# Optimization experiments

Hardware: AMD Instinct MI355X
Metric: run time of the kernel (lower is better)

## Reference

```python
import jax, jax.numpy as jnp
import numpy as np

MARGIN = 0.3  # hard-coded in all three MarginRankingLoss instances


def setup_inputs() -> dict:
    key = jax.random.key(0)
    k1, k2, k3, k4 = jax.random.split(key, 4)
    n, d, num_ids = 4096, 2048, 100
    inputs = jax.random.normal(k1, (n, d), dtype=jnp.float32)
    targets_a = jax.random.randint(k2, (n,), 0, num_ids, dtype=jnp.int64)
    targets_b = jax.random.randint(k3, (n,), 0, num_ids, dtype=jnp.int64)
    lam = jax.random.uniform(k4, (), dtype=jnp.float32)
    epoch = 60
    return {"inputs": inputs, "targets_a": targets_a, "targets_b": targets_b,
            "lam": lam, "epoch": epoch}


def reference(inputs, targets_a, targets_b, lam, epoch):
    # pairwise euclidean distance: dist[i,j] = ||x_i - x_j||
    sq = jnp.sum(inputs * inputs, axis=1)                      # [n]
    dist = sq[:, None] + sq[None, :] - 2.0 * (inputs @ inputs.T)
    dist = jnp.sqrt(jnp.clip(dist, 1e-12))                     # [n, n]

    ma = targets_a[:, None] == targets_a[None, :]
    mb = targets_b[:, None] == targets_b[None, :]
    m_same_ab = ma & mb                                        # same a AND b (incl. diagonal)
    m_same_or = (ma & ~mb) | (~ma & mb)                        # exactly one of a/b matches
    m_dif_ab = ~ma & ~mb                                       # neither matches

    ninf = -jnp.inf
    pinf = jnp.inf
    hp = jnp.max(jnp.where(m_same_ab, dist, ninf), axis=1)     # hardest positive
    hn = jnp.min(jnp.where(m_dif_ab, dist, pinf), axis=1)      # hardest negative
    max_or = jnp.max(jnp.where(m_same_or, dist, ninf), axis=1)
    min_or = jnp.min(jnp.where(m_same_or, dist, pinf), axis=1)

    use_or = m_same_or.any(axis=1) & (epoch > 50)
    sp = jnp.where(use_or, max_or, hp)
    sn = jnp.where(use_or, min_or, hn)

    # MarginRankingLoss(x1, x2, y=1) = mean(relu(x2 - x1 + margin))
    loss_1 = jnp.mean(jnp.maximum(0.0, hp - hn + MARGIN))
    loss_2 = jnp.mean(jnp.maximum(0.0, sp - hn + MARGIN))
    loss_3 = jnp.mean(jnp.maximum(0.0, hp - sn + MARGIN))
    return loss_1 + loss_2 + loss_3
```

## Files before the change

kernel.cpp:

```cpp
#include <hip/hip_runtime.h>
#include <hip/hip_bf16.h>

#define NROW 4096
#define KDIM 2048
#define ROWB (KDIM * 2)
#define BT 256
#define BK 64
#define NT (KDIM / BK)
#define LDSBUF 65536
#define PHI(r) (((r) & 7) << 4)

typedef __attribute__((ext_vector_type(8))) short bf16x8;
typedef __attribute__((ext_vector_type(4))) float f32x4;
typedef __attribute__((ext_vector_type(4))) unsigned short u16x4;

#define MFMA16(a, b, c) __builtin_amdgcn_mfma_f32_16x16x32_bf16((a), (b), (c), 0, 0, 0)

__device__ __forceinline__ unsigned short f2bf(float x) {
    unsigned u = __float_as_uint(x);
    unsigned r = (u + 0x7FFFu + ((u >> 16) & 1u)) >> 16;
    return (unsigned short)r;
}
__device__ __forceinline__ float bf2f(unsigned short b) {
    return __uint_as_float(((unsigned)b) << 16);
}

__global__ __launch_bounds__(256) void k_convert(const float* __restrict__ X,
                                                 unsigned short* __restrict__ Xb,
                                                 float* __restrict__ sqv) {
    const int row = blockIdx.x;
    const int t = threadIdx.x;
    const float4* xr = (const float4*)(X + (size_t)row * KDIM);
    unsigned short* br = Xb + (size_t)row * KDIM;
    float acc = 0.f;
#pragma unroll
    for (int it = 0; it < 2; ++it) {
        int idx = t * 2 + it;
        float4 v = xr[idx];
        u16x4 b;
        b.x = f2bf(v.x); b.y = f2bf(v.y); b.z = f2bf(v.z); b.w = f2bf(v.w);
        float f0 = bf2f(b.x), f1 = bf2f(b.y), f2 = bf2f(b.z), f3 = bf2f(b.w);
        acc += f0 * f0 + f1 * f1 + f2 * f2 + f3 * f3;
        *(u16x4*)(br + idx * 4) = b;
    }
#pragma unroll
    for (int s = 32; s > 0; s >>= 1) acc += __shfl_xor(acc, s);
    __shared__ float red[4];
    const int lane = t & 63, wid = t >> 6;
    if (lane == 0) red[wid] = acc;
    __syncthreads();
    if (t == 0) sqv[row] = red[0] + red[1] + red[2] + red[3];
}

__global__ __launch_bounds__(256) void k_init(unsigned* hp, unsigned* hn,
                                              unsigned* mor, unsigned* mir,
                                              int* anyor, float* out) {
    int i = blockIdx.x * 256 + threadIdx.x;
    hp[i] = 0u;
    hn[i] = 0x7F800000u;
    mor[i] = 0u;
    mir[i] = 0x7F800000u;
    anyor[i] = 0;
    if (i == 0) out[0] = 0.f;
}

__global__ __launch_bounds__(512, 2) void k_gemm(const unsigned short* __restrict__ Xb,
                                                 const float* __restrict__ sqv,
                                                 const int* __restrict__ ta,
                                                 const int* __restrict__ tb,
                                                 unsigned int* __restrict__ hp,
                                                 unsigned int* __restrict__ hn,
                                                 unsigned int* __restrict__ mor,
                                                 unsigned int* __restrict__ mir,
                                                 int* __restrict__ anyor) {
    __shared__ char lds[2 * LDSBUF];
    const int bi = blockIdx.x >> 4;
    const int bj = blockIdx.x & 15;
    const int t = threadIdx.x;
    const int lane = t & 63;
    const int w = t >> 6;
    const int wm = w >> 2;
    const int wn = w & 3;
    const int l15 = lane & 15;
    const int kg16 = (lane >> 4) * 16;
    const char* xbase = (const char*)Xb;

    const int P = (l15 & 7) << 4;
    int akb[2], bkb[2];
#pragma unroll
    for (int ks = 0; ks < 2; ++ks) {
        const int kx = (ks * 64 + kg16) ^ P;
        akb[ks] = (wm * 128 + l15) * 128 + kx;
        bkb[ks] = 32768 + (wn * 64 + l15) * 128 + kx;
    }

    f32x4 acc[8][4] = {};

#define STAGE(tt, p)                                                          \
    do {                                                                      \
        constexpr int isb_ = (p) >= 4;                                        \
        constexpr int c_ = (p) - isb_ * 4;                                    \
        const int row_ = c_ * 64 + (t >> 3);                                  \
        const int gr_ = (isb_ ? bj : bi) * BT + row_;                         \
        const char* gsrc_ = xbase + (size_t)gr_ * ROWB + (size_t)(tt) * 128 + \
                            (((t & 7) * 16) ^ PHI(row_));                     \
        char* ldst_ = lds + ((tt) & 1) * LDSBUF + isb_ * 32768 + row_ * 128 + \
                      (t & 7) * 16;                                           \
        __builtin_amdgcn_global_load_lds(                                     \
            (const __attribute__((address_space(1))) void*)gsrc_,             \
            (__attribute__((address_space(3))) void*)ldst_, 16, 0, 0);        \
    } while (0)

    STAGE(0, 0); STAGE(0, 2); STAGE(0, 4); STAGE(0, 5);
    STAGE(0, 6); STAGE(0, 7); STAGE(0, 1); STAGE(0, 3);
    asm volatile("s_waitcnt vmcnt(2)" ::: "memory");
    __builtin_amdgcn_s_barrier();

    bf16x8 af0[4][2], af1[4][2], b01[2][2], b23[2][2];
#pragma unroll
    for (int ks = 0; ks < 2; ++ks) {
#pragma unroll
        for (int m = 0; m < 4; ++m)
            af0[m][ks] = *(const bf16x8*)(lds + akb[ks] + m * 2048);
        b01[0][ks] = *(const bf16x8*)(lds + bkb[ks]);
        b01[1][ks] = *(const bf16x8*)(lds + bkb[ks] + 2048);
    }

    for (int tk = 0; tk < NT; ++tk) {
        const char* bufc = lds + (tk & 1) * LDSBUF;
        const char* bufn = lds + ((tk + 1) & 1) * LDSBUF;
        const bool stg = (tk + 1) < NT;

        if (stg) {
            STAGE(tk + 1, 0); STAGE(tk + 1, 2); STAGE(tk + 1, 4);
            STAGE(tk + 1, 5); STAGE(tk + 1, 6); STAGE(tk + 1, 7);
        }
#pragma unroll
        for (int ks = 0; ks < 2; ++ks) {
            b23[0][ks] = *(const bf16x8*)(bufc + bkb[ks] + 2 * 2048);
            b23[1][ks] = *(const bf16x8*)(bufc + bkb[ks] + 3 * 2048);
        }
        __builtin_amdgcn_s_setprio(1);
#pragma unroll
        for (int ks = 0; ks < 2; ++ks)
#pragma unroll
            for (int m = 0; m < 4; ++m) {
                acc[m][0] = MFMA16(af0[m][ks], b01[0][ks], acc[m][0]);
                acc[m][1] = MFMA16(af0[m][ks], b01[1][ks], acc[m][1]);
            }
        __builtin_amdgcn_s_setprio(0);

        if (stg) {
            STAGE(tk + 1, 1); STAGE(tk + 1, 3);
            asm volatile("s_waitcnt vmcnt(8)" ::: "memory");
        } else {
            asm volatile("s_waitcnt vmcnt(0)" ::: "memory");
        }
        __builtin_amdgcn_s_barrier();
#pragma unroll
        for (int ks = 0; ks < 2; ++ks)
#pragma unroll
            for (int m = 0; m < 4; ++m)
                af1[m][ks] = *(const bf16x8*)(bufc + akb[ks] + (4 + m) * 2048);
        __builtin_amdgcn_s_setprio(1);
#pragma unroll
        for (int ks = 0; ks < 2; ++ks)
#pragma unroll
            for (int m = 0; m < 4; ++m) {
                acc[m][2] = MFMA16(af0[m][ks], b23[0][ks], acc[m][2]);
                acc[m][3] = MFMA16(af0[m][ks], b23[1][ks], acc[m][3]);
            }
        __builtin_amdgcn_s_setprio(0);

        if (stg) {
            asm volatile("s_waitcnt vmcnt(2)" ::: "memory");
            __builtin_amdgcn_s_barrier();
#pragma unroll
            for (int ks = 0; ks < 2; ++ks)
#pragma unroll
                for (int m = 0; m < 4; ++m)
                    af0[m][ks] = *(const bf16x8*)(bufn + akb[ks] + m * 2048);
        }
        __builtin_amdgcn_s_setprio(1);
#pragma unroll
        for (int ks = 0; ks < 2; ++ks)
#pragma unroll
            for (int m = 0; m < 4; ++m) {
                acc[4 + m][2] = MFMA16(af1[m][ks], b23[0][ks], acc[4 + m][2]);
                acc[4 + m][3] = MFMA16(af1[m][ks], b23[1][ks], acc[4 + m][3]);
            }
        __builtin_amdgcn_s_setprio(0);

        __builtin_amdgcn_s_setprio(1);
#pragma unroll
        for (int ks = 0; ks < 2; ++ks)
#pragma unroll
            for (int m = 0; m < 4; ++m) {
                acc[4 + m][0] = MFMA16(af1[m][ks], b01[0][ks], acc[4 + m][0]);
                acc[4 + m][1] = MFMA16(af1[m][ks], b01[1][ks], acc[4 + m][1]);
            }
        __builtin_amdgcn_s_setprio(0);
        if (stg) {
#pragma unroll
            for (int ks = 0; ks < 2; ++ks) {
                b01[0][ks] = *(const bf16x8*)(bufn + bkb[ks]);
                b01[1][ks] = *(const bf16x8*)(bufn + bkb[ks] + 2048);
            }
        }
        __builtin_amdgcn_s_barrier();
    }
#undef STAGE

    float sqj[4];
    int taj[4], tbj[4];
#pragma unroll
    for (int n = 0; n < 4; ++n) {
        int j = bj * BT + wn * 64 + n * 16 + l15;
        sqj[n] = sqv[j];
        taj[n] = ta[j];
        tbj[n] = tb[j];
    }
    const float INF = __uint_as_float(0x7F800000u);
#pragma unroll
    for (int m = 0; m < 8; ++m) {
#pragma unroll
        for (int reg = 0; reg < 4; ++reg) {
            const int i = bi * BT + wm * 128 + m * 16 + (lane >> 4) * 4 + reg;
            const float sqi = sqv[i];
            const int tai = ta[i], tbi = tb[i];
            float vhp = 0.f, vhn = INF, vmor = 0.f, vmir = INF, vany = 0.f;
#pragma unroll
            for (int n = 0; n < 4; ++n) {
                float d2 = sqi + sqj[n] - 2.f * acc[m][n][reg];
                float d = sqrtf(fmaxf(d2, 1e-12f));
                bool ma = (tai == taj[n]), mb = (tbi == tbj[n]);
                if (ma && mb) {
                    vhp = fmaxf(vhp, d);
                } else if (ma != mb) {
                    vmor = fmaxf(vmor, d);
                    vmir = fminf(vmir, d);
                    vany = 1.f;
                } else {
                    vhn = fminf(vhn, d);
                }
            }
#pragma unroll
            for (int s = 1; s < 16; s <<= 1) {
                vhp = fmaxf(vhp, __shfl_xor(vhp, s, 16));
                vhn = fminf(vhn, __shfl_xor(vhn, s, 16));
                vmor = fmaxf(vmor, __shfl_xor(vmor, s, 16));
                vmir = fminf(vmir, __shfl_xor(vmir, s, 16));
                vany = fmaxf(vany, __shfl_xor(vany, s, 16));
            }
            if (l15 == 0) {
                if (vhp > 0.f) atomicMax(&hp[i], __float_as_uint(vhp));
                if (vhn < INF) atomicMin(&hn[i], __float_as_uint(vhn));
                if (vany > 0.f) {
                    atomicMax(&mor[i], __float_as_uint(vmor));
                    atomicMin(&mir[i], __float_as_uint(vmir));
                    atomicOr(&anyor[i], 1);
                }
            }
        }
    }
}

__global__ __launch_bounds__(256) void k_final(const unsigned* __restrict__ hp,
                                               const unsigned* __restrict__ hn,
                                               const unsigned* __restrict__ mor,
                                               const unsigned* __restrict__ mir,
                                               const int* __restrict__ anyor,
                                               const int* __restrict__ epoch_p,
                                               float* __restrict__ out) {
    const int t = threadIdx.x;
    const int i = blockIdx.x * 256 + t;
    const bool eok = (*epoch_p > 50);
    float fhp = __uint_as_float(hp[i]);
    float fhn = __uint_as_float(hn[i]);
    bool use_or = (anyor[i] != 0) && eok;
    float sp = use_or ? __uint_as_float(mor[i]) : fhp;
    float sn = use_or ? __uint_as_float(mir[i]) : fhn;
    float s = fmaxf(0.f, fhp - fhn + 0.3f) + fmaxf(0.f, sp - fhn + 0.3f) +
              fmaxf(0.f, fhp - sn + 0.3f);
#pragma unroll
    for (int sh = 32; sh > 0; sh >>= 1) s += __shfl_xor(s, sh);
    __shared__ float red[4];
    const int lane = t & 63, wid = t >> 6;
    if (lane == 0) red[wid] = s;
    __syncthreads();
    if (t == 0)
        atomicAdd(out, (red[0] + red[1] + red[2] + red[3]) * (1.f / 4096.f));
}

extern "C" void kernel_launch(void* const* d_in, const int* in_sizes, int n_in,
                              void* d_out, int out_size, void* d_ws, size_t ws_size,
                              hipStream_t stream) {
    const float* X = (const float*)d_in[0];
    const int* ta = (const int*)d_in[1];
    const int* tb = (const int*)d_in[2];
    const int* epoch_p = (const int*)d_in[4];
    float* out = (float*)d_out;

    char* ws = (char*)d_ws;
    unsigned short* Xb = (unsigned short*)ws;
    size_t off = (size_t)NROW * KDIM * sizeof(unsigned short);
    float* sqv = (float*)(ws + off); off += (size_t)NROW * 4;
    unsigned* hp = (unsigned*)(ws + off); off += (size_t)NROW * 4;
    unsigned* hn = (unsigned*)(ws + off); off += (size_t)NROW * 4;
    unsigned* mor = (unsigned*)(ws + off); off += (size_t)NROW * 4;
    unsigned* mir = (unsigned*)(ws + off); off += (size_t)NROW * 4;
    int* anyor = (int*)(ws + off); off += (size_t)NROW * 4;

    k_convert<<<NROW, 256, 0, stream>>>(X, Xb, sqv);
    k_init<<<NROW / 256, 256, 0, stream>>>(hp, hn, mor, mir, anyor, out);
    k_gemm<<<(NROW / BT) * (NROW / BT), 512, 0, stream>>>(Xb, sqv, ta, tb,
                                                          hp, hn, mor, mir, anyor);
    k_final<<<NROW / 256, 256, 0, stream>>>(hp, hn, mor, mir, anyor, epoch_p, out);
}
```

Measured before the change: 108.2 us.

## Restructure GEMM main loop into two-tile unrolled ping-pong with per-phase barriers

The K loop is unrolled over two K tiles per iteration, with both LDS buffers prefetched at the start. Global-to-LDS staging is split into half-tile chunks interleaved between the four MFMA phases. Each phase is fenced by sched_barrier, s_barrier and lgkmcnt waits in the style of an AMD ping-pong schedule. The goal is to hide memory latency and balance LDS reads against MFMA work, but the extra barriers add synchronisation cost. The wrap-around index (masking with NKT-1) also issues redundant loads of tiles 0 and 1 in the last iteration.

```diff
diff --git a/kernel.cpp b/kernel.cpp
--- a/kernel.cpp
+++ b/kernel.cpp
@@ -6,7 +6,8 @@
 #define ROWB (KDIM * 2)
 #define BT 256
 #define BK 64
-#define NT (KDIM / BK)
+#define NKT (KDIM / BK)
+#define ITERS (NKT / 2)
 #define LDSBUF 65536
 #define PHI(r) (((r) & 7) << 4)
 
@@ -96,51 +97,57 @@
 
     f32x4 acc[8][4] = {};
 
-#define STAGE(tt, p)                                                          \
+#define STAGEH(kt_, isb_, hh_)                                                \
     do {                                                                      \
-        constexpr int isb_ = (p) >= 4;                                        \
-        constexpr int c_ = (p) - isb_ * 4;                                    \
-        const int row_ = c_ * 64 + (t >> 3);                                  \
-        const int gr_ = (isb_ ? bj : bi) * BT + row_;                         \
-        const char* gsrc_ = xbase + (size_t)gr_ * ROWB + (size_t)(tt) * 128 + \
-                            (((t & 7) * 16) ^ PHI(row_));                     \
-        char* ldst_ = lds + ((tt) & 1) * LDSBUF + isb_ * 32768 + row_ * 128 + \
-                      (t & 7) * 16;                                           \
-        __builtin_amdgcn_global_load_lds(                                     \
-            (const __attribute__((address_space(1))) void*)gsrc_,             \
-            (__attribute__((address_space(3))) void*)ldst_, 16, 0, 0);        \
+        _Pragma("unroll")                                                     \
+        for (int q_ = 0; q_ < 2; ++q_) {                                      \
+            const int row_ = (hh_) * 128 + q_ * 64 + (t >> 3);                \
+            const int gr_ = ((isb_) ? bj : bi) * BT + row_;                   \
+            const char* gsrc_ = xbase + (size_t)gr_ * ROWB +                  \
+                                (size_t)(kt_) * 128 +                         \
+                                (((t & 7) * 16) ^ PHI(row_));                 \
+            char* ldst_ = lds + ((kt_) & 1) * LDSBUF + (isb_) * 32768 +       \
+                          row_ * 128 + (t & 7) * 16;                          \
+            __builtin_amdgcn_global_load_lds(                                 \
+                (const __attribute__((address_space(1))) void*)gsrc_,         \
+                (__attribute__((address_space(3))) void*)ldst_, 16, 0, 0);    \
+        }                                                                     \
     } while (0)
 
-    STAGE(0, 0); STAGE(0, 2); STAGE(0, 4); STAGE(0, 5);
-    STAGE(0, 6); STAGE(0, 7); STAGE(0, 1); STAGE(0, 3);
-    asm volatile("s_waitcnt vmcnt(2)" ::: "memory");
+#define SYNC_PRE                                                              \
+    __builtin_amdgcn_sched_barrier(0);                                        \
+    __builtin_amdgcn_s_barrier();                                             \
+    asm volatile("s_waitcnt lgkmcnt(0)" ::: "memory");                        \
+    __builtin_amdgcn_sched_barrier(0);                                        \
+    __builtin_amdgcn_s_setprio(1);
+
+#define SYNC_POST                                                             \
+    __builtin_amdgcn_s_setprio(0);                                            \
+    __builtin_amdgcn_sched_barrier(0);                                        \
     __builtin_amdgcn_s_barrier();
 
+    STAGEH(0, 0, 0); STAGEH(0, 0, 1); STAGEH(0, 1, 0); STAGEH(0, 1, 1);
+    STAGEH(1, 0, 0); STAGEH(1, 0, 1); STAGEH(1, 1, 0); STAGEH(1, 1, 1);
+    asm volatile("s_waitcnt vmcnt(8)" ::: "memory");
+    __builtin_amdgcn_s_barrier();
+
     bf16x8 af0[4][2], af1[4][2], b01[2][2], b23[2][2];
-#pragma unroll
-    for (int ks = 0; ks < 2; ++ks) {
-#pragma unroll
-        for (int m = 0; m < 4; ++m)
-            af0[m][ks] = *(const bf16x8*)(lds + akb[ks] + m * 2048);
-        b01[0][ks] = *(const bf16x8*)(lds + bkb[ks]);
-        b01[1][ks] = *(const bf16x8*)(lds + bkb[ks] + 2048);
-    }
-
-    for (int tk = 0; tk < NT; ++tk) {
-        const char* bufc = lds + (tk & 1) * LDSBUF;
-        const char* bufn = lds + ((tk + 1) & 1) * LDSBUF;
-        const bool stg = (tk + 1) < NT;
-
-        if (stg) {
-            STAGE(tk + 1, 0); STAGE(tk + 1, 2); STAGE(tk + 1, 4);
-            STAGE(tk + 1, 5); STAGE(tk + 1, 6); STAGE(tk + 1, 7);
-        }
+    const char* buf0 = lds;
+    const char* buf1 = lds + LDSBUF;
+
+    for (int it = 0; it < ITERS; ++it) {
+        const int nk0 = (2 * it + 2) & (NKT - 1);
+        const int nk1 = (2 * it + 3) & (NKT - 1);
+
 #pragma unroll
         for (int ks = 0; ks < 2; ++ks) {
-            b23[0][ks] = *(const bf16x8*)(bufc + bkb[ks] + 2 * 2048);
-            b23[1][ks] = *(const bf16x8*)(bufc + bkb[ks] + 3 * 2048);
-        }
-        __builtin_amdgcn_s_setprio(1);
+#pragma unroll
+            for (int m = 0; m < 4; ++m)
+                af0[m][ks] = *(const bf16x8*)(buf0 + akb[ks] + m * 2048);
+            b01[0][ks] = *(const bf16x8*)(buf0 + bkb[ks]);
+            b01[1][ks] = *(const bf16x8*)(buf0 + bkb[ks] + 2048);
+        }
+        SYNC_PRE
 #pragma unroll
         for (int ks = 0; ks < 2; ++ks)
 #pragma unroll
@@ -148,21 +155,14 @@
                 acc[m][0] = MFMA16(af0[m][ks], b01[0][ks], acc[m][0]);
                 acc[m][1] = MFMA16(af0[m][ks], b01[1][ks], acc[m][1]);
             }
-        __builtin_amdgcn_s_setprio(0);
-
-        if (stg) {
-            STAGE(tk + 1, 1); STAGE(tk + 1, 3);
-            asm volatile("s_waitcnt vmcnt(8)" ::: "memory");
-        } else {
-            asm volatile("s_waitcnt vmcnt(0)" ::: "memory");
-        }
-        __builtin_amdgcn_s_barrier();
-#pragma unroll
-        for (int ks = 0; ks < 2; ++ks)
-#pragma unroll
-            for (int m = 0; m < 4; ++m)
-                af1[m][ks] = *(const bf16x8*)(bufc + akb[ks] + (4 + m) * 2048);
-        __builtin_amdgcn_s_setprio(1);
+        SYNC_POST
+
+#pragma unroll
+        for (int ks = 0; ks < 2; ++ks) {
+            b23[0][ks] = *(const bf16x8*)(buf0 + bkb[ks] + 2 * 2048);
+            b23[1][ks] = *(const bf16x8*)(buf0 + bkb[ks] + 3 * 2048);
+        }
+        SYNC_PRE
 #pragma unroll
         for (int ks = 0; ks < 2; ++ks)
 #pragma unroll
@@ -170,18 +170,14 @@
                 acc[m][2] = MFMA16(af0[m][ks], b23[0][ks], acc[m][2]);
                 acc[m][3] = MFMA16(af0[m][ks], b23[1][ks], acc[m][3]);
             }
-        __builtin_amdgcn_s_setprio(0);
-
-        if (stg) {
-            asm volatile("s_waitcnt vmcnt(2)" ::: "memory");
-            __builtin_amdgcn_s_barrier();
-#pragma unroll
-            for (int ks = 0; ks < 2; ++ks)
-#pragma unroll
-                for (int m = 0; m < 4; ++m)
-                    af0[m][ks] = *(const bf16x8*)(bufn + akb[ks] + m * 2048);
-        }
-        __builtin_amdgcn_s_setprio(1);
+        SYNC_POST
+
+#pragma unroll
+        for (int ks = 0; ks < 2; ++ks)
+#pragma unroll
+            for (int m = 0; m < 4; ++m)
+                af1[m][ks] = *(const bf16x8*)(buf0 + akb[ks] + (4 + m) * 2048);
+        SYNC_PRE
 #pragma unroll
         for (int ks = 0; ks < 2; ++ks)
 #pragma unroll
@@ -189,9 +185,10 @@
                 acc[4 + m][2] = MFMA16(af1[m][ks], b23[0][ks], acc[4 + m][2]);
                 acc[4 + m][3] = MFMA16(af1[m][ks], b23[1][ks], acc[4 + m][3]);
             }
-        __builtin_amdgcn_s_setprio(0);
-
-        __builtin_amdgcn_s_setprio(1);
+        SYNC_POST
+
+        asm volatile("s_waitcnt vmcnt(0)" ::: "memory");
+        SYNC_PRE
 #pragma unroll
         for (int ks = 0; ks < 2; ++ks)
 #pragma unroll
@@ -199,17 +196,75 @@
                 acc[4 + m][0] = MFMA16(af1[m][ks], b01[0][ks], acc[4 + m][0]);
                 acc[4 + m][1] = MFMA16(af1[m][ks], b01[1][ks], acc[4 + m][1]);
             }
-        __builtin_amdgcn_s_setprio(0);
-        if (stg) {
-#pragma unroll
-            for (int ks = 0; ks < 2; ++ks) {
-                b01[0][ks] = *(const bf16x8*)(bufn + bkb[ks]);
-                b01[1][ks] = *(const bf16x8*)(bufn + bkb[ks] + 2048);
-            }
-        }
-        __builtin_amdgcn_s_barrier();
-    }
-#undef STAGE
+        SYNC_POST
+
+#pragma unroll
+        for (int ks = 0; ks < 2; ++ks) {
+#pragma unroll
+            for (int m = 0; m < 4; ++m)
+                af0[m][ks] = *(const bf16x8*)(buf1 + akb[ks] + m * 2048);
+            b01[0][ks] = *(const bf16x8*)(buf1 + bkb[ks]);
+            b01[1][ks] = *(const bf16x8*)(buf1 + bkb[ks] + 2048);
+        }
+        STAGEH(nk0, 0, 0); STAGEH(nk0, 0, 1);
+        SYNC_PRE
+#pragma unroll
+        for (int ks = 0; ks < 2; ++ks)
+#pragma unroll
+            for (int m = 0; m < 4; ++m) {
+                acc[m][0] = MFMA16(af0[m][ks], b01[0][ks], acc[m][0]);
+                acc[m][1] = MFMA16(af0[m][ks], b01[1][ks], acc[m][1]);
+            }
+        SYNC_POST
+
+#pragma unroll
+        for (int ks = 0; ks < 2; ++ks) {
+            b23[0][ks] = *(const bf16x8*)(buf1 + bkb[ks] + 2 * 2048);
+            b23[1][ks] = *(const bf16x8*)(buf1 + bkb[ks] + 3 * 2048);
+        }
+        STAGEH(nk0, 1, 0); STAGEH(nk0, 1, 1);
+        SYNC_PRE
+#pragma unroll
+        for (int ks = 0; ks < 2; ++ks)
+#pragma unroll
+            for (int m = 0; m < 4; ++m) {
+                acc[m][2] = MFMA16(af0[m][ks], b23[0][ks], acc[m][2]);
+                acc[m][3] = MFMA16(af0[m][ks], b23[1][ks], acc[m][3]);
+            }
+        SYNC_POST
+
+#pragma unroll
+        for (int ks = 0; ks < 2; ++ks)
+#pragma unroll
+            for (int m = 0; m < 4; ++m)
+                af1[m][ks] = *(const bf16x8*)(buf1 + akb[ks] + (4 + m) * 2048);
+        STAGEH(nk1, 1, 0); STAGEH(nk1, 1, 1);
+        SYNC_PRE
+#pragma unroll
+        for (int ks = 0; ks < 2; ++ks)
+#pragma unroll
+            for (int m = 0; m < 4; ++m) {
+                acc[4 + m][2] = MFMA16(af1[m][ks], b23[0][ks], acc[4 + m][2]);
+                acc[4 + m][3] = MFMA16(af1[m][ks], b23[1][ks], acc[4 + m][3]);
+            }
+        SYNC_POST
+
+        STAGEH(nk1, 0, 0); STAGEH(nk1, 0, 1);
+        asm volatile("s_waitcnt vmcnt(8)" ::: "memory");
+        SYNC_PRE
+#pragma unroll
+        for (int ks = 0; ks < 2; ++ks)
+#pragma unroll
+            for (int m = 0; m < 4; ++m) {
+                acc[4 + m][0] = MFMA16(af1[m][ks], b01[0][ks], acc[4 + m][0]);
+                acc[4 + m][1] = MFMA16(af1[m][ks], b01[1][ks], acc[4 + m][1]);
+            }
+        SYNC_POST
+    }
+    asm volatile("s_waitcnt vmcnt(0)" ::: "memory");
+#undef STAGEH
+#undef SYNC_PRE
+#undef SYNC_POST
 
     float sqj[4];
     int taj[4], tbj[4];
```

After: 144.8 us. 1.34x slower.
